# Optimization experiments

Measured on AMD Instinct MI355X. Metric: run time of the kernel, lower is better.

Reference implementation:

```python
import jax, jax.numpy as jnp
import numpy as np

N_NODES = 100000

def _scatter_mean(vals, idx, num_segments):
    # vals: [E, D], idx: [E] -> [num_segments, D], mean with zero-degree -> 0 (PyG clamps count to 1)
    s = jax.ops.segment_sum(vals, idx, num_segments=num_segments)
    cnt = jax.ops.segment_sum(jnp.ones((vals.shape[0],), vals.dtype), idx, num_segments=num_segments)
    return s / jnp.maximum(cnt, 1.0)[:, None]

def _conv(x, edge_index, W1, W2, Wr, br):
    src, dst = edge_index[0], edge_index[1]
    n = x.shape[0]
    # flow source_to_target: aggregate lin1(x)[src] at dst
    out1 = _scatter_mean((x @ W1)[src], dst, n)
    # flow target_to_source: aggregate lin2(x)[dst] at src
    out2 = _scatter_mean((x @ W2)[dst], src, n)
    return x @ Wr + br + out1 + out2

def setup_inputs() -> dict:
    key = jax.random.key(0)
    ks = jax.random.split(key, 10)
    d_in, d_h, E = 64, 64, 1250000
    x = jax.random.normal(ks[0], (N_NODES, d_in), dtype=jnp.float32)
    edge_index = jax.random.randint(ks[1], (2, E), 0, N_NODES)
    def lin(k, fan_in, fan_out):
        bound = 1.0 / np.sqrt(fan_in)
        return jax.random.uniform(k, (fan_in, fan_out), jnp.float32, -bound, bound)
    inp = {"x": x, "edge_index": edge_index}
    inp["W1_0"] = lin(ks[2], d_in, d_h)
    inp["W2_0"] = lin(ks[3], d_in, d_h)
    inp["Wr_0"] = lin(ks[4], d_in, d_h)
    inp["br_0"] = jax.random.uniform(ks[5], (d_h,), jnp.float32, -1/np.sqrt(d_in), 1/np.sqrt(d_in))
    inp["W1_1"] = lin(ks[6], d_h, d_h)
    inp["W2_1"] = lin(ks[7], d_h, d_h)
    inp["Wr_1"] = lin(ks[8], d_h, d_h)
    inp["br_1"] = jax.random.uniform(ks[9], (d_h,), jnp.float32, -1/np.sqrt(d_h), 1/np.sqrt(d_h))
    return inp

def reference(x, edge_index, W1_0, W2_0, Wr_0, br_0, W1_1, W2_1, Wr_1, br_1):
    h = jax.nn.relu(_conv(x, edge_index, W1_0, W2_0, Wr_0, br_0))
    h = jax.nn.relu(_conv(h, edge_index, W1_1, W2_1, Wr_1, br_1))
    return h
```

## Files before the change

kernel.cpp:

```cpp
#include <hip/hip_runtime.h>


typedef __bf16 bf16x8 __attribute__((ext_vector_type(8)));
typedef float  f32x4  __attribute__((ext_vector_type(4)));

#define BSHIFT 9
#define NBMAX  256
#define CAPLOG 13
#define CAP    (1 << CAPLOG)

__launch_bounds__(256)
__global__ void k_bin(const int* __restrict__ ei, int E,
                      int* __restrict__ gcnt ,
                      unsigned* __restrict__ binbuf ) {
    __shared__ int lcnt[2 * NBMAX];
    const int tid = threadIdx.x;
    lcnt[tid] = 0; lcnt[NBMAX + tid] = 0;
    __syncthreads();
    const int start = blockIdx.x * 8192;
    const int end = min(start + 8192, E);
    for (int e = start + tid; e < end; e += 256) {
        int s = ei[e], d = ei[E + e];
        atomicAdd(&lcnt[d >> BSHIFT], 1);
        atomicAdd(&lcnt[NBMAX + (s >> BSHIFT)], 1);
    }
    __syncthreads();
    {
        int c0 = lcnt[tid], c1 = lcnt[NBMAX + tid];
        int b0 = c0 ? atomicAdd(&gcnt[tid], c0) : 0;
        int b1 = c1 ? atomicAdd(&gcnt[NBMAX + tid], c1) : 0;
        lcnt[tid] = b0; lcnt[NBMAX + tid] = b1;
    }
    __syncthreads();
    for (int e = start + tid; e < end; e += 256) {
        int s = ei[e], d = ei[E + e];
        int bi = d >> BSHIFT;
        int p = atomicAdd(&lcnt[bi], 1);
        if (p < CAP)
            binbuf[(bi << CAPLOG) + p] = ((unsigned)(d & 511) << 17) | (unsigned)s;
        int bo = s >> BSHIFT;
        int p2 = atomicAdd(&lcnt[NBMAX + bo], 1);
        if (p2 < CAP)
            binbuf[((NBMAX + bo) << CAPLOG) + p2] = ((unsigned)(s & 511) << 17) | (unsigned)d;
    }
}

__launch_bounds__(256)
__global__ void k_binfill2(const unsigned* __restrict__ binbuf, const int* __restrict__ gcnt,
                           int n,
                           int* __restrict__ rp_in, int* __restrict__ rp_out,
                           int* __restrict__ ci_in, int* __restrict__ ci_out) {
    __shared__ int h[512];
    __shared__ int cur[512];
    __shared__ int gb[NBMAX];
    __shared__ int s_tot;
    const int dir = blockIdx.y, bkt = blockIdx.x, tid = threadIdx.x;
    int* rp = dir ? rp_out : rp_in;
    int* ci = dir ? ci_out : ci_in;
    h[tid] = 0; h[256 + tid] = 0;
    gb[tid] = gcnt[dir * NBMAX + tid];
    __syncthreads();
    for (int off = 1; off < NBMAX; off <<= 1) {
        int t = (tid >= off) ? gb[tid - off] : 0;
        __syncthreads();
        gb[tid] += t;
        __syncthreads();
    }
    const int base_off = bkt ? gb[bkt - 1] : 0;
    const int cnt = min(gcnt[dir * NBMAX + bkt], CAP);
    const unsigned* buf = binbuf + (((size_t)dir * NBMAX + bkt) << CAPLOG);
    for (int i = tid; i < cnt; i += 256)
        atomicAdd(&h[buf[i] >> 17], 1);
    __syncthreads();
    for (int d = 1; d < 512; d <<= 1) {
        int idx = (tid + 1) * (d << 1) - 1;
        if (idx < 512) h[idx] += h[idx - d];
        __syncthreads();
    }
    if (tid == 0) { s_tot = h[511]; h[511] = 0; }
    __syncthreads();
    for (int d = 256; d >= 1; d >>= 1) {
        int idx = (tid + 1) * (d << 1) - 1;
        if (idx < 512) { int t = h[idx - d]; h[idx - d] = h[idx]; h[idx] += t; }
        __syncthreads();
    }
    const int nodebase = bkt << BSHIFT;
    for (int i = tid; i < 512; i += 256) {
        int nd = nodebase + i;
        int v = base_off + h[i];
        cur[i] = v;
        if (nd < n) rp[nd] = v;
    }
    if (tid == 0 && ((n - 1) >> BSHIFT) == bkt)
        rp[n] = base_off + s_tot;
    __syncthreads();
    for (int i = tid; i < cnt; i += 256) {
        unsigned ent = buf[i];
        int slot = atomicAdd(&cur[ent >> 17], 1);
        ci[slot] = (int)(ent & 0x1FFFFu);
    }
}

__global__ void k_prep2(const float* __restrict__ W1a, const float* __restrict__ W2a,
                        const float* __restrict__ Wra,
                        __bf16* __restrict__ WcTha, __bf16* __restrict__ WcTla,
                        __bf16* __restrict__ WrTha, __bf16* __restrict__ WrTla,
                        const float* __restrict__ W1b, const float* __restrict__ W2b,
                        const float* __restrict__ Wrb,
                        __bf16* __restrict__ WcThb, __bf16* __restrict__ WcTlb,
                        __bf16* __restrict__ WrThb, __bf16* __restrict__ WrTlb) {
    const float *W1, *W2, *Wr;
    __bf16 *Wch, *Wcl, *Wrh, *Wrl;
    if (blockIdx.y == 0) { W1 = W1a; W2 = W2a; Wr = Wra; Wch = WcTha; Wcl = WcTla; Wrh = WrTha; Wrl = WrTla; }
    else                 { W1 = W1b; W2 = W2b; Wr = Wrb; Wch = WcThb; Wcl = WcTlb; Wrh = WrThb; Wrl = WrTlb; }
    int i = blockIdx.x * 256 + threadIdx.x;
    if (i < 8192) {
        int nn = i >> 7, k = i & 127;
        float w = (k < 64) ? W1[k * 64 + nn] : W2[(k - 64) * 64 + nn];
        __bf16 h = (__bf16)w;
        Wch[i] = h;
        Wcl[i] = (__bf16)(w - (float)h);
    } else if (i < 12288) {
        int j = i - 8192;
        int nn = j >> 6, k = j & 63;
        float w = Wr[k * 64 + nn];
        __bf16 h = (__bf16)w;
        Wrh[j] = h;
        Wrl[j] = (__bf16)(w - (float)h);
    }
}

__launch_bounds__(256, 6)
__global__ void k_gather(const float* __restrict__ Hin,
                         const int* __restrict__ rp_in, const int* __restrict__ ci_in,
                         const int* __restrict__ rp_out, const int* __restrict__ ci_out,
                         __bf16* __restrict__ Ah, __bf16* __restrict__ Al, int n) {
    const int lane = threadIdx.x & 63;
    const int wid  = threadIdx.x >> 6;
    const int v = blockIdx.x * 4 + wid;
    if (v >= n) return;
    const int q = lane & 15, sub = lane >> 4;

    const int s0 = rp_in[v],  e0 = rp_in[v + 1],  len0 = e0 - s0;
    const int s1 = rp_out[v], e1 = rp_out[v + 1], len1 = e1 - s1;
    const int mlen = max(len0, len1);
    const float* __restrict__ hq = Hin + q * 4;

    float4 a0 = {0.f, 0.f, 0.f, 0.f}, a1 = {0.f, 0.f, 0.f, 0.f};
    for (int t = sub; t < mlen; t += 16) {
        #pragma unroll
        for (int u = 0; u < 4; ++u) {
            int r = t + u * 4;
            if (r < len0) {
                int nd = ci_in[s0 + r];
                float4 f = *(const float4*)(hq + (size_t)nd * 64);
                a0.x += f.x; a0.y += f.y; a0.z += f.z; a0.w += f.w;
            }
            if (r < len1) {
                int nd = ci_out[s1 + r];
                float4 f = *(const float4*)(hq + (size_t)nd * 64);
                a1.x += f.x; a1.y += f.y; a1.z += f.z; a1.w += f.w;
            }
        }
    }
    #pragma unroll
    for (int m = 16; m <= 32; m <<= 1) {
        a0.x += __shfl_xor(a0.x, m, 64); a0.y += __shfl_xor(a0.y, m, 64);
        a0.z += __shfl_xor(a0.z, m, 64); a0.w += __shfl_xor(a0.w, m, 64);
        a1.x += __shfl_xor(a1.x, m, 64); a1.y += __shfl_xor(a1.y, m, 64);
        a1.z += __shfl_xor(a1.z, m, 64); a1.w += __shfl_xor(a1.w, m, 64);
    }
    float inv0 = 1.0f / (float)max(len0, 1);
    float inv1 = 1.0f / (float)max(len1, 1);
    a0.x *= inv0; a0.y *= inv0; a0.z *= inv0; a0.w *= inv0;
    a1.x *= inv1; a1.y *= inv1; a1.z *= inv1; a1.w *= inv1;

    if (sub == 0) {
        #pragma unroll
        for (int dir = 0; dir < 2; ++dir) {
            float m[4] = {dir ? a1.x : a0.x, dir ? a1.y : a0.y,
                          dir ? a1.z : a0.z, dir ? a1.w : a0.w};
            union { __bf16 h[4]; uint2 u2; } ph, pl;
            #pragma unroll
            for (int c = 0; c < 4; ++c) {
                __bf16 h = (__bf16)m[c];
                ph.h[c] = h;
                pl.h[c] = (__bf16)(m[c] - (float)h);
            }
            size_t off = (size_t)v * 128 + dir * 64 + q * 4;
            *(uint2*)(Ah + off) = ph.u2;
            *(uint2*)(Al + off) = pl.u2;
        }
    }
}

__global__ void k_gemm(const __bf16* __restrict__ Ah, const __bf16* __restrict__ Al,
                       const float* __restrict__ Hin,
                       const __bf16* __restrict__ WcT_h, const __bf16* __restrict__ WcT_l,
                       const __bf16* __restrict__ WrT_h, const __bf16* __restrict__ WrT_l,
                       const float* __restrict__ br, float* __restrict__ Hout, int n) {
    const int lane = threadIdx.x & 63;
    const int wid  = threadIdx.x >> 6;
    const int q = lane & 15, sub = lane >> 4;
    const int rowbase = blockIdx.x * 64 + wid * 16;
    const int arow = min(rowbase + q, n - 1);

    f32x4 acc[4];
    #pragma unroll
    for (int nf = 0; nf < 4; ++nf) acc[nf] = (f32x4){0.f, 0.f, 0.f, 0.f};

    #pragma unroll
    for (int ks = 0; ks < 4; ++ks) {
        const size_t ao = (size_t)arow * 128 + ks * 32 + sub * 8;
        bf16x8 a_h = *(const bf16x8*)(Ah + ao);
        bf16x8 a_l = *(const bf16x8*)(Al + ao);
        #pragma unroll
        for (int nf = 0; nf < 4; ++nf) {
            const size_t bo = (size_t)(nf * 16 + q) * 128 + ks * 32 + sub * 8;
            bf16x8 b_h = *(const bf16x8*)(WcT_h + bo);
            bf16x8 b_l = *(const bf16x8*)(WcT_l + bo);
            acc[nf] = __builtin_amdgcn_mfma_f32_16x16x32_bf16(a_h, b_h, acc[nf], 0, 0, 0);
            acc[nf] = __builtin_amdgcn_mfma_f32_16x16x32_bf16(a_h, b_l, acc[nf], 0, 0, 0);
            acc[nf] = __builtin_amdgcn_mfma_f32_16x16x32_bf16(a_l, b_h, acc[nf], 0, 0, 0);
        }
    }
    #pragma unroll
    for (int ks = 0; ks < 2; ++ks) {
        const float* hp = Hin + (size_t)arow * 64 + ks * 32 + sub * 8;
        float4 h0 = *(const float4*)hp;
        float4 h1 = *(const float4*)(hp + 4);
        float hf[8] = {h0.x, h0.y, h0.z, h0.w, h1.x, h1.y, h1.z, h1.w};
        bf16x8 a_h, a_l;
        #pragma unroll
        for (int c = 0; c < 8; ++c) {
            __bf16 h = (__bf16)hf[c];
            a_h[c] = h;
            a_l[c] = (__bf16)(hf[c] - (float)h);
        }
        #pragma unroll
        for (int nf = 0; nf < 4; ++nf) {
            const size_t bo = (size_t)(nf * 16 + q) * 64 + ks * 32 + sub * 8;
            bf16x8 b_h = *(const bf16x8*)(WrT_h + bo);
            bf16x8 b_l = *(const bf16x8*)(WrT_l + bo);
            acc[nf] = __builtin_amdgcn_mfma_f32_16x16x32_bf16(a_h, b_h, acc[nf], 0, 0, 0);
            acc[nf] = __builtin_amdgcn_mfma_f32_16x16x32_bf16(a_h, b_l, acc[nf], 0, 0, 0);
            acc[nf] = __builtin_amdgcn_mfma_f32_16x16x32_bf16(a_l, b_h, acc[nf], 0, 0, 0);
        }
    }
    #pragma unroll
    for (int nf = 0; nf < 4; ++nf) {
        int col = nf * 16 + q;
        float b = br[col];
        #pragma unroll
        for (int reg = 0; reg < 4; ++reg) {
            int row = rowbase + sub * 4 + reg;
            if (row < n)
                Hout[(size_t)row * 64 + col] = fmaxf(acc[nf][reg] + b, 0.f);
        }
    }
}

extern "C" void kernel_launch(void* const* d_in, const int* in_sizes, int n_in,
                              void* d_out, int out_size, void* d_ws, size_t ws_size,
                              hipStream_t stream) {
    const float* x    = (const float*)d_in[0];
    const int*   ei   = (const int*)d_in[1];
    const float* W1_0 = (const float*)d_in[2];
    const float* W2_0 = (const float*)d_in[3];
    const float* Wr_0 = (const float*)d_in[4];
    const float* br_0 = (const float*)d_in[5];
    const float* W1_1 = (const float*)d_in[6];
    const float* W2_1 = (const float*)d_in[7];
    const float* Wr_1 = (const float*)d_in[8];
    const float* br_1 = (const float*)d_in[9];
    float* out = (float*)d_out;

    const int N = in_sizes[0] / 64;
    const int E = in_sizes[1] / 2;
    const int NB = (N + 511) >> BSHIFT;

    char* p = (char*)d_ws;
    auto alloc = [&](size_t bytes) { char* r = p; p += (bytes + 255) & ~255ULL; return r; };

    int* rp_in   = (int*)alloc(((size_t)N + 1) * 4);
    int* rp_out  = (int*)alloc(((size_t)N + 1) * 4);
    int* gcnt    = (int*)alloc(2 * NBMAX * 4);
    int* ci_in   = (int*)alloc((size_t)E * 4);
    int* ci_out  = (int*)alloc((size_t)E * 4);
    __bf16* Ah   = (__bf16*)alloc((size_t)N * 128 * 2);
    __bf16* Al   = (__bf16*)alloc((size_t)N * 128 * 2);
    float* H     = (float*)alloc((size_t)N * 64 * 4);
    __bf16* WcT_h0 = (__bf16*)alloc(8192 * 2);
    __bf16* WcT_l0 = (__bf16*)alloc(8192 * 2);
    __bf16* WrT_h0 = (__bf16*)alloc(4096 * 2);
    __bf16* WrT_l0 = (__bf16*)alloc(4096 * 2);
    __bf16* WcT_h1 = (__bf16*)alloc(8192 * 2);
    __bf16* WcT_l1 = (__bf16*)alloc(8192 * 2);
    __bf16* WrT_h1 = (__bf16*)alloc(4096 * 2);
    __bf16* WrT_l1 = (__bf16*)alloc(4096 * 2);

    unsigned* binbuf = (unsigned*)Ah;

    hipMemsetAsync(gcnt, 0, 2 * NBMAX * 4, stream);

    int bb = (E + 8191) / 8192;
    k_bin<<<bb, 256, 0, stream>>>(ei, E, gcnt, binbuf);
    k_binfill2<<<dim3(NB, 2), 256, 0, stream>>>(binbuf, gcnt, N,
                                                rp_in, rp_out, ci_in, ci_out);
    k_prep2<<<dim3(48, 2), 256, 0, stream>>>(W1_0, W2_0, Wr_0, WcT_h0, WcT_l0, WrT_h0, WrT_l0,
                                             W1_1, W2_1, Wr_1, WcT_h1, WcT_l1, WrT_h1, WrT_l1);

    int gb = (N + 3) / 4;
    int mb = (N + 63) / 64;

    k_gather<<<gb, 256, 0, stream>>>(x, rp_in, ci_in, rp_out, ci_out, Ah, Al, N);
    k_gemm<<<mb, 256, 0, stream>>>(Ah, Al, x, WcT_h0, WcT_l0, WrT_h0, WrT_l0, br_0, H, N);

    k_gather<<<gb, 256, 0, stream>>>(H, rp_in, ci_in, rp_out, ci_out, Ah, Al, N);
    k_gemm<<<mb, 256, 0, stream>>>(Ah, Al, H, WcT_h1, WcT_l1, WrT_h1, WrT_l1, br_1, out, N);
}
```

Baseline: 442.3 us.

## Gather neighbor features from fp16 copy and restructure per-direction gather loop

Node features are converted to an fp16 copy (a new conversion kernel for x, and the first GEMM writes an fp16 copy of its output), so the irregular neighbor gather reads half the bytes per edge. The gather loop now handles each direction separately with 8-edge unrolled steps, and occupancy is raised to 8 waves per SIMD. The trade-offs are an extra conversion pass and an extra fp16 store, plus lower precision on the gathered features, which could affect accuracy tolerance.

```diff
diff --git a/kernel.cpp b/kernel.cpp
--- a/kernel.cpp
+++ b/kernel.cpp
@@ -3,6 +3,7 @@
 
 typedef __bf16 bf16x8 __attribute__((ext_vector_type(8)));
 typedef float  f32x4  __attribute__((ext_vector_type(4)));
+typedef _Float16 half4 __attribute__((ext_vector_type(4)));
 
 #define BSHIFT 9
 #define NBMAX  256
@@ -130,8 +131,16 @@
     }
 }
 
-__launch_bounds__(256, 6)
-__global__ void k_gather(const float* __restrict__ Hin,
+__global__ void k_tohalf(const float* __restrict__ X, _Float16* __restrict__ F, int n64) {
+    int i = (blockIdx.x * 256 + threadIdx.x) * 4;
+    if (i >= n64) return;
+    float4 v = *(const float4*)(X + i);
+    half4 h = { (_Float16)v.x, (_Float16)v.y, (_Float16)v.z, (_Float16)v.w };
+    *(half4*)(F + i) = h;
+}
+
+__launch_bounds__(256, 8)
+__global__ void k_gather(const _Float16* __restrict__ F,
                          const int* __restrict__ rp_in, const int* __restrict__ ci_in,
                          const int* __restrict__ rp_out, const int* __restrict__ ci_out,
                          __bf16* __restrict__ Ah, __bf16* __restrict__ Al, int n) {
@@ -140,47 +149,43 @@
     const int v = blockIdx.x * 4 + wid;
     if (v >= n) return;
     const int q = lane & 15, sub = lane >> 4;
-
-    const int s0 = rp_in[v],  e0 = rp_in[v + 1],  len0 = e0 - s0;
-    const int s1 = rp_out[v], e1 = rp_out[v + 1], len1 = e1 - s1;
-    const int mlen = max(len0, len1);
-    const float* __restrict__ hq = Hin + q * 4;
-
-    float4 a0 = {0.f, 0.f, 0.f, 0.f}, a1 = {0.f, 0.f, 0.f, 0.f};
-    for (int t = sub; t < mlen; t += 16) {
-        #pragma unroll
-        for (int u = 0; u < 4; ++u) {
-            int r = t + u * 4;
-            if (r < len0) {
-                int nd = ci_in[s0 + r];
-                float4 f = *(const float4*)(hq + (size_t)nd * 64);
-                a0.x += f.x; a0.y += f.y; a0.z += f.z; a0.w += f.w;
+    const _Float16* __restrict__ fq = F + q * 4;
+
+    #pragma unroll
+    for (int dir = 0; dir < 2; ++dir) {
+        const int* rp = dir ? rp_out : rp_in;
+        const int* ci = dir ? ci_out : ci_in;
+        int s = rp[v], e = rp[v + 1];
+        float ax = 0.f, ay = 0.f, az = 0.f, aw = 0.f;
+        int t = s;
+        for (; t + 8 <= e; t += 8) {
+            int u0 = ci[t + sub];
+            int u1 = ci[t + 4 + sub];
+            half4 f0 = *(const half4*)(fq + (size_t)u0 * 64);
+            half4 f1 = *(const half4*)(fq + (size_t)u1 * 64);
+            ax += (float)f0[0] + (float)f1[0];
+            ay += (float)f0[1] + (float)f1[1];
+            az += (float)f0[2] + (float)f1[2];
+            aw += (float)f0[3] + (float)f1[3];
+        }
+        for (; t < e; t += 4) {
+            int r = t + sub;
+            if (r < e) {
+                half4 f = *(const half4*)(fq + (size_t)ci[r] * 64);
+                ax += (float)f[0]; ay += (float)f[1];
+                az += (float)f[2]; aw += (float)f[3];
             }
-            if (r < len1) {
-                int nd = ci_out[s1 + r];
-                float4 f = *(const float4*)(hq + (size_t)nd * 64);
-                a1.x += f.x; a1.y += f.y; a1.z += f.z; a1.w += f.w;
-            }
-        }
-    }
-    #pragma unroll
-    for (int m = 16; m <= 32; m <<= 1) {
-        a0.x += __shfl_xor(a0.x, m, 64); a0.y += __shfl_xor(a0.y, m, 64);
-        a0.z += __shfl_xor(a0.z, m, 64); a0.w += __shfl_xor(a0.w, m, 64);
-        a1.x += __shfl_xor(a1.x, m, 64); a1.y += __shfl_xor(a1.y, m, 64);
-        a1.z += __shfl_xor(a1.z, m, 64); a1.w += __shfl_xor(a1.w, m, 64);
-    }
-    float inv0 = 1.0f / (float)max(len0, 1);
-    float inv1 = 1.0f / (float)max(len1, 1);
-    a0.x *= inv0; a0.y *= inv0; a0.z *= inv0; a0.w *= inv0;
-    a1.x *= inv1; a1.y *= inv1; a1.z *= inv1; a1.w *= inv1;
-
-    if (sub == 0) {
-        #pragma unroll
-        for (int dir = 0; dir < 2; ++dir) {
-            float m[4] = {dir ? a1.x : a0.x, dir ? a1.y : a0.y,
-                          dir ? a1.z : a0.z, dir ? a1.w : a0.w};
+        }
+        ax += __shfl_xor(ax, 16, 64); ax += __shfl_xor(ax, 32, 64);
+        ay += __shfl_xor(ay, 16, 64); ay += __shfl_xor(ay, 32, 64);
+        az += __shfl_xor(az, 16, 64); az += __shfl_xor(az, 32, 64);
+        aw += __shfl_xor(aw, 16, 64); aw += __shfl_xor(aw, 32, 64);
+        float inv = 1.0f / (float)max(e - s, 1);
+        ax *= inv; ay *= inv; az *= inv; aw *= inv;
+
+        if (sub == 0) {
             union { __bf16 h[4]; uint2 u2; } ph, pl;
+            float m[4] = {ax, ay, az, aw};
             #pragma unroll
             for (int c = 0; c < 4; ++c) {
                 __bf16 h = (__bf16)m[c];
@@ -198,7 +203,8 @@
                        const float* __restrict__ Hin,
                        const __bf16* __restrict__ WcT_h, const __bf16* __restrict__ WcT_l,
                        const __bf16* __restrict__ WrT_h, const __bf16* __restrict__ WrT_l,
-                       const float* __restrict__ br, float* __restrict__ Hout, int n) {
+                       const float* __restrict__ br, float* __restrict__ Hout,
+                       _Float16* __restrict__ Fout, int n) {
     const int lane = threadIdx.x & 63;
     const int wid  = threadIdx.x >> 6;
     const int q = lane & 15, sub = lane >> 4;
@@ -254,8 +260,11 @@
         #pragma unroll
         for (int reg = 0; reg < 4; ++reg) {
             int row = rowbase + sub * 4 + reg;
-            if (row < n)
-                Hout[(size_t)row * 64 + col] = fmaxf(acc[nf][reg] + b, 0.f);
+            if (row < n) {
+                float val = fmaxf(acc[nf][reg] + b, 0.f);
+                Hout[(size_t)row * 64 + col] = val;
+                if (Fout) Fout[(size_t)row * 64 + col] = (_Float16)val;
+            }
         }
     }
 }
@@ -290,6 +299,7 @@
     __bf16* Ah   = (__bf16*)alloc((size_t)N * 128 * 2);
     __bf16* Al   = (__bf16*)alloc((size_t)N * 128 * 2);
     float* H     = (float*)alloc((size_t)N * 64 * 4);
+    _Float16* F  = (_Float16*)alloc((size_t)N * 64 * 2);
     __bf16* WcT_h0 = (__bf16*)alloc(8192 * 2);
     __bf16* WcT_l0 = (__bf16*)alloc(8192 * 2);
     __bf16* WrT_h0 = (__bf16*)alloc(4096 * 2);
@@ -309,13 +319,15 @@
                                                 rp_in, rp_out, ci_in, ci_out);
     k_prep2<<<dim3(48, 2), 256, 0, stream>>>(W1_0, W2_0, Wr_0, WcT_h0, WcT_l0, WrT_h0, WrT_l0,
                                              W1_1, W2_1, Wr_1, WcT_h1, WcT_l1, WrT_h1, WrT_l1);
+    k_tohalf<<<(N * 64 / 4 + 255) / 256, 256, 0, stream>>>(x, F, N * 64);
 
     int gb = (N + 3) / 4;
     int mb = (N + 63) / 64;
 
-    k_gather<<<gb, 256, 0, stream>>>(x, rp_in, ci_in, rp_out, ci_out, Ah, Al, N);
-    k_gemm<<<mb, 256, 0, stream>>>(Ah, Al, x, WcT_h0, WcT_l0, WrT_h0, WrT_l0, br_0, H, N);
-
-    k_gather<<<gb, 256, 0, stream>>>(H, rp_in, ci_in, rp_out, ci_out, Ah, Al, N);
-    k_gemm<<<mb, 256, 0, stream>>>(Ah, Al, H, WcT_h1, WcT_l1, WrT_h1, WrT_l1, br_1, out, N);
-}
+    k_gather<<<gb, 256, 0, stream>>>(F, rp_in, ci_in, rp_out, ci_out, Ah, Al, N);
+    k_gemm<<<mb, 256, 0, stream>>>(Ah, Al, x, WcT_h0, WcT_l0, WrT_h0, WrT_l0, br_0, H, F, N);
+
+    k_gather<<<gb, 256, 0, stream>>>(F, rp_in, ci_in, rp_out, ci_out, Ah, Al, N);
+    k_gemm<<<mb, 256, 0, stream>>>(Ah, Al, H, WcT_h1, WcT_l1, WrT_h1, WrT_l1, br_1, out,
+                                   (_Float16*)nullptr, N);
+}
```

New measurement: 402.8 us. 8.9% less time.
